# Kernel optimization log

Measured on AMD Instinct MI355X. Metric: run time of the kernel, lower is better.

## Reference

```python
import jax, jax.numpy as jnp
import numpy as np

N_PTILES = 4096
MAX_SOURCES = 1
PTILE_SLEN = 53  # odd -> slen == ptile_slen, size_lens is identity
N_BANDS = 1


def setup_inputs() -> dict:
    key = jax.random.key(0)
    k1, k2, k3, k4, k5, k6 = jax.random.split(key, 6)
    shape = (N_PTILES, MAX_SOURCES)
    gal = jax.random.uniform(k1, shape + (7,), dtype=jnp.float32)
    # realistic SIE lens params per _sample_lens_params: b in [5,30], q in (0,1)
    b = jax.random.uniform(k2, shape + (1,), dtype=jnp.float32) * 25.0 + 5.0
    centers = jax.random.normal(k3, shape + (2,), dtype=jnp.float32)
    q = jax.random.uniform(k4, shape + (1,), dtype=jnp.float32) * 0.8 + 0.1
    beta = (jax.random.uniform(k5, shape + (1,), dtype=jnp.float32) - 0.5) * (np.pi / 2)
    ellf = (1.0 - q) / (1.0 + q)
    e1 = ellf * jnp.cos(beta)
    e2 = ellf * jnp.sin(beta)
    lens_params = jnp.concatenate([gal, b, centers, e1, e2], axis=-1)  # [..., 12]
    bools = (jax.random.uniform(k6, shape + (1,), dtype=jnp.float32) < 0.7).astype(jnp.float32)
    return {"lens_params": lens_params, "lensed_galaxy_bools": bools}


def _render_unlensed(gal_p, slen):
    # Differentiable Gaussian stand-in for the (CPU galsim) unlensed source render.
    c = jnp.arange(slen, dtype=jnp.float32) - (slen - 1) / 2.0
    yy, xx = jnp.meshgrid(c, c, indexing="ij")
    flux = gal_p[:, 0] * 1000.0 + 100.0      # [N]
    sigma = gal_p[:, 3] * 3.0 + 1.0          # [N]
    r2 = xx[None] ** 2 + yy[None] ** 2       # [1, S, S]
    s2 = (sigma ** 2)[:, None, None]
    return flux[:, None, None] * jnp.exp(-0.5 * r2 / s2) / (2.0 * np.pi * s2)


def _sie_deflection(x, y, lens_p):
    # x, y: [1, S, S]; lens_p: [N, 5] -> (xg, yg): [N, S, S]
    b, cx, cy, e1, e2 = [lens_p[:, i][:, None, None] for i in range(5)]
    ell = jnp.sqrt(e1 ** 2 + e2 ** 2)
    q = (1.0 - ell) / (1.0 + ell)
    phirad = jnp.arctan(e2 / e1)
    cosp, sinp = jnp.cos(phirad), jnp.sin(phirad)
    xsie = (x - cx) * cosp + (y - cy) * sinp
    ysie = (y - cy) * cosp - (x - cx) * sinp
    r_ell = jnp.sqrt(q * xsie ** 2 + ysie ** 2 / q + 1e-12)
    qfact = jnp.sqrt(1.0 / q - q)
    eps = 0.001
    safe = jnp.maximum(qfact, eps)
    denom = r_ell + (r_ell == 0)
    xtg = jnp.where(qfact >= eps, b / safe * jnp.arctan(safe * xsie / denom), b * xsie / denom)
    ytg = jnp.where(qfact >= eps, b / safe * jnp.arctanh(safe * ysie / denom), b * ysie / denom)
    xg = xtg * cosp - ytg * sinp
    yg = ytg * cosp + xtg * sinp
    return xg, yg


def _bilinear(im, xs, ys):
    # im: [N, S, S]; xs (col coord), ys (row coord): [N, S, S]
    N, S, _ = im.shape
    x0 = jnp.clip(jnp.floor(xs).astype(jnp.int32), 0, S - 1)
    x1 = jnp.clip(jnp.floor(xs).astype(jnp.int32) + 1, 0, S - 1)
    y0 = jnp.clip(jnp.floor(ys).astype(jnp.int32), 0, S - 1)
    y1 = jnp.clip(jnp.floor(ys).astype(jnp.int32) + 1, 0, S - 1)
    flat = im.reshape(N, S * S)

    def g(yi, xi):
        return jnp.take_along_axis(flat, (yi * S + xi).reshape(N, -1), axis=1).reshape(N, S, S)

    x0f, x1f = x0.astype(im.dtype), x1.astype(im.dtype)
    y0f, y1f = y0.astype(im.dtype), y1.astype(im.dtype)
    # weights use the CLIPPED integer corners, matching bilinear_interpolate_numpy
    wa = (x1f - xs) * (y1f - ys)
    wb = (x1f - xs) * (ys - y0f)
    wc = (xs - x0f) * (y1f - ys)
    wd = (xs - x0f) * (ys - y0f)
    return g(y0, x0) * wa + g(y1, x0) * wb + g(y0, x1) * wc + g(y1, x1) * wd


def _forward(lens_params, lensed_galaxy_bools):
    n_ptiles, max_s, P = lens_params.shape
    z = lens_params.reshape(-1, P)
    gal_p, lens_p = z[:, :7], z[:, 7:]
    slen = PTILE_SLEN
    unlensed = _render_unlensed(gal_p, slen)            # [N, S, S]
    # grid exactly as lens_galsim: range [-nx//2, nx//2] over nx points
    nx = slen
    lo = float((-nx) // 2)   # -27 for nx=53
    hi = float(nx // 2)      # 26
    coords = (hi - lo) * jnp.arange(nx, dtype=jnp.float32) / (nx - 1) + lo
    x = jnp.broadcast_to(coords[None, :], (nx, nx))  # varies along columns
    y = jnp.broadcast_to(coords[:, None], (nx, nx))  # varies along rows
    xg, yg = _sie_deflection(x[None], y[None], lens_p)
    shift = float(nx // 2)
    lensed = _bilinear(unlensed, x[None] - xg + shift, y[None] - yg + shift)
    out = lensed.reshape(n_ptiles, max_s, N_BANDS, slen, slen)
    # render-all + mask is equivalent to the zeros-init + boolean-fill + final mask
    return out * lensed_galaxy_bools[..., None, None]


def reference(lens_params, lensed_galaxy_bools):
    return _forward(lens_params, lensed_galaxy_bools)
```

## Files before the change

kernel.cpp:

```cpp
#include <hip/hip_runtime.h>
#include <math.h>

#define SLEN 53
#define NPIX (SLEN * SLEN)
#define NPARAM 12
#define BLK 256
#define NITER ((NPIX + BLK - 1) / BLK)

__device__ __forceinline__ float fast_atan(float u) {
    float t = __builtin_fabsf(u);
    float rin = __builtin_amdgcn_rcpf(t);
    bool big = t > 1.0f;
    float w = big ? rin : t;
    bool mid = w > 0.4142135624f;
    float w2 = (w - 1.0f) * __builtin_amdgcn_rcpf(w + 1.0f);
    float x = mid ? w2 : w;
    float z = x * x;
    float p = ((8.05374449538e-2f * z - 1.38776856032e-1f) * z
               + 1.99777106478e-1f) * z - 3.33329491539e-1f;
    float r = __builtin_fmaf(p * z, x, x);
    r = mid ? r + 0.78539816339744831f : r;
    r = big ? 1.57079632679489662f - r : r;
    return __builtin_copysignf(r, u);
}

__device__ __forceinline__ float fast_atanh(float v) {
    float a = __builtin_fabsf(v);
    float r = 0.34657359027997264f *
              (__builtin_amdgcn_logf(1.0f + a) - __builtin_amdgcn_logf(1.0f - a));
    return __builtin_copysignf(r, v);
}

__global__ __launch_bounds__(BLK) void lgtd_kernel(
    const float* __restrict__ lens_params,
    const float* __restrict__ bools,
    float* __restrict__ out)
{
    const int tile = blockIdx.x;
    float* outp = out + (size_t)tile * NPIX;
    const int tid = threadIdx.x;

    const float bl = bools[tile];
    if (bl == 0.0f) {
        int idx = tid;
        #pragma unroll
        for (int it = 0; it < NITER; ++it, idx += BLK)
            if (it < NITER - 1 || idx < NPIX) outp[idx] = 0.0f;
        return;
    }

    const float* p = lens_params + tile * NPARAM;
    const float flux  = p[0] * 1000.0f + 100.0f;
    const float sigma = p[3] * 3.0f + 1.0f;
    const float s2    = sigma * sigma;
    const float A     = bl * flux / (6.28318530717958647692f * s2);
    const float nh2   = -0.5f / s2 * 1.44269504088896340736f;
    const float b  = p[7];
    const float cx = p[8], cy = p[9];
    const float e1 = p[10], e2 = p[11];
    const float ell    = sqrtf(e1 * e1 + e2 * e2);
    const float q      = (1.0f - ell) / (1.0f + ell);
    const float qinv   = 1.0f / q;
    const float phirad = atanf(e2 / e1);
    const float cosp   = cosf(phirad);
    const float sinp   = sinf(phirad);
    const float qfact  = sqrtf(qinv - q);
    const float eps    = 0.001f;
    const float safe   = fmaxf(qfact, eps);
    const float bos    = b / safe;
    const bool  main_branch = (qfact >= eps);

    __shared__ float Ctab[SLEN];
    __shared__ float Etab[SLEN];
    if (tid < SLEN) {
        const float kf = (float)tid;
        Ctab[tid] = 53.0f * kf / 52.0f - 27.0f;
        const float d = kf - 26.0f;
        Etab[tid] = __builtin_amdgcn_exp2f(nh2 * (d * d));
    }
    __syncthreads();

    int idx = tid;
    #pragma unroll
    for (int it = 0; it < NITER; ++it, idx += BLK) {
        if (it == NITER - 1 && idx >= NPIX) break;
        const int i = idx / SLEN;
        const int j = idx - i * SLEN;
        const float xc = Ctab[j];
        const float yc = Ctab[i];

        const float dx = xc - cx, dy = yc - cy;
        const float xsie = dx * cosp + dy * sinp;
        const float ysie = dy * cosp - dx * sinp;
        const float arg = q * xsie * xsie + qinv * ysie * ysie + 1e-12f;
        const float rcp_r = __builtin_amdgcn_rsqf(arg);
        float xtg, ytg;
        if (main_branch) {
            xtg = bos * fast_atan(safe * xsie * rcp_r);
            ytg = bos * fast_atanh(safe * ysie * rcp_r);
        } else {
            xtg = b * xsie * rcp_r;
            ytg = b * ysie * rcp_r;
        }
        const float xg = xtg * cosp - ytg * sinp;
        const float yg = ytg * cosp + xtg * sinp;

        const float xs = (xc - xg) + 26.0f;
        const float ys = (yc - yg) + 26.0f;
        const int x0i = (int)floorf(xs), y0i = (int)floorf(ys);
        const int x0 = min(max(x0i,     0), SLEN - 1);
        const int x1 = min(max(x0i + 1, 0), SLEN - 1);
        const int y0 = min(max(y0i,     0), SLEN - 1);
        const int y1 = min(max(y0i + 1, 0), SLEN - 1);
        const float x0f = (float)x0, x1f = (float)x1;
        const float y0f = (float)y0, y1f = (float)y1;

        const float Fx = (x1f - xs) * Etab[x0] + (xs - x0f) * Etab[x1];
        const float Fy = (y1f - ys) * Etab[y0] + (ys - y0f) * Etab[y1];
        outp[idx] = A * Fx * Fy;
    }
}

extern "C" void kernel_launch(void* const* d_in, const int* in_sizes, int n_in,
                              void* d_out, int out_size, void* d_ws, size_t ws_size,
                              hipStream_t stream) {
    const float* lens  = (const float*)d_in[0];
    const float* bools = (const float*)d_in[1];
    float* out = (float*)d_out;
    const int n_tiles = in_sizes[1];
    lgtd_kernel<<<n_tiles, BLK, 0, stream>>>(lens, bools, out);
}
```

Before: 88.07 us.

## Split per-tile parameter prep into separate kernel and batch pixel work

Moves the per-tile scalar setup (atan, cos, sin, sqrt, divisions) into a small prep kernel that writes a 16-float record per tile to workspace. The main kernel reads that record and templates the pixel loop on the deflection branch. It processes pixels in groups of four so loads and stores can overlap with math. It also replaces the divide by 53 with a multiply-shift, does the clamping in float, and computes atanh with one log and a reciprocal. The cost is an extra kernel launch and a workspace round trip, and the one-log atanh may differ slightly in accuracy.

```diff
diff --git a/kernel.cpp b/kernel.cpp
--- a/kernel.cpp
+++ b/kernel.cpp
@@ -2,10 +2,11 @@
 #include <math.h>
 
 #define SLEN 53
-#define NPIX (SLEN * SLEN)
+#define NPIX 2809
 #define NPARAM 12
 #define BLK 256
-#define NITER ((NPIX + BLK - 1) / BLK)
+#define PW 16
+#define NSLOT 11
 
 __device__ __forceinline__ float fast_atan(float u) {
     float t = __builtin_fabsf(u);
@@ -26,49 +27,130 @@
 
 __device__ __forceinline__ float fast_atanh(float v) {
     float a = __builtin_fabsf(v);
-    float r = 0.34657359027997264f *
-              (__builtin_amdgcn_logf(1.0f + a) - __builtin_amdgcn_logf(1.0f - a));
+    float t = (1.0f + a) * __builtin_amdgcn_rcpf(1.0f - a);
+    float r = 0.34657359027997264f * __builtin_amdgcn_logf(t);
     return __builtin_copysignf(r, v);
 }
 
-__global__ __launch_bounds__(BLK) void lgtd_kernel(
+__global__ __launch_bounds__(BLK) void prep_kernel(
     const float* __restrict__ lens_params,
     const float* __restrict__ bools,
+    float* __restrict__ ws, int n_tiles)
+{
+    int t = blockIdx.x * blockDim.x + threadIdx.x;
+    if (t >= n_tiles) return;
+    const float* p = lens_params + t * NPARAM;
+    const float bl   = bools[t];
+    const float flux = p[0] * 1000.0f + 100.0f;
+    const float sg   = p[3] * 3.0f + 1.0f;
+    const float s2   = sg * sg;
+    const float A    = bl * flux / (6.28318530717958647692f * s2);
+    const float nh2  = -0.5f / s2 * 1.44269504088896340736f;
+    const float b  = p[7], cx = p[8], cy = p[9], e1 = p[10], e2 = p[11];
+    const float ell  = sqrtf(e1 * e1 + e2 * e2);
+    const float q    = (1.0f - ell) / (1.0f + ell);
+    const float qinv = 1.0f / q;
+    const float ph   = atanf(e2 / e1);
+    const float cosp = cosf(ph), sinp = sinf(ph);
+    const float qf   = sqrtf(qinv - q);
+    const float safe = fmaxf(qf, 0.001f);
+    const float bos  = b / safe;
+    float* w = ws + t * PW;
+    w[0]  = bl;   w[1]  = A;    w[2]  = nh2;  w[3]  = cosp;
+    w[4]  = sinp; w[5]  = q;    w[6]  = qinv; w[7]  = safe;
+    w[8]  = bos;  w[9]  = cx;   w[10] = cy;   w[11] = b;
+    w[12] = (qf >= 0.001f) ? 1.0f : 0.0f;
+    w[13] = 0.0f; w[14] = 0.0f; w[15] = 0.0f;
+}
+
+template<bool MB>
+__device__ __forceinline__ void run_tile(
+    float* __restrict__ outp, int tid,
+    const float* __restrict__ Ctab, const float* __restrict__ Etab,
+    float A, float cosp, float sinp, float q, float qinv,
+    float safe, float bos, float cx, float cy, float b)
+{
+    #pragma unroll
+    for (int g = 0; g < 3; ++g) {
+        const int nk = (g == 2) ? 3 : 4;
+        float xc[4], yc[4], val[4];
+        #pragma unroll
+        for (int k = 0; k < 4; ++k) {
+            if (k >= nk) break;
+            const int slot = g * 4 + k;
+            int idx = slot * BLK + tid;
+            if (slot == NSLOT - 1) idx = min(idx, NPIX - 1);
+            const unsigned i = ((unsigned)idx * 39569u) >> 21;
+            const int j = idx - (int)i * 53;
+            xc[k] = Ctab[j];
+            yc[k] = Ctab[i];
+        }
+        #pragma unroll
+        for (int k = 0; k < 4; ++k) {
+            if (k >= nk) break;
+            const float dx = xc[k] - cx, dy = yc[k] - cy;
+            const float xsie = dx * cosp + dy * sinp;
+            const float ysie = dy * cosp - dx * sinp;
+            const float arg = __builtin_fmaf(q * xsie, xsie,
+                              __builtin_fmaf(qinv * ysie, ysie, 1e-12f));
+            const float rcp_r = __builtin_amdgcn_rsqf(arg);
+            float xtg, ytg;
+            if (MB) {
+                xtg = bos * fast_atan(safe * xsie * rcp_r);
+                ytg = bos * fast_atanh(safe * ysie * rcp_r);
+            } else {
+                xtg = b * xsie * rcp_r;
+                ytg = b * ysie * rcp_r;
+            }
+            const float xg = xtg * cosp - ytg * sinp;
+            const float yg = ytg * cosp + xtg * sinp;
+            const float xs = (xc[k] - xg) + 26.0f;
+            const float ys = (yc[k] - yg) + 26.0f;
+            const float fx = __builtin_floorf(xs);
+            const float fy = __builtin_floorf(ys);
+            const float x0f = fminf(fmaxf(fx, 0.0f), 52.0f);
+            const float x1f = fminf(fmaxf(fx + 1.0f, 0.0f), 52.0f);
+            const float y0f = fminf(fmaxf(fy, 0.0f), 52.0f);
+            const float y1f = fminf(fmaxf(fy + 1.0f, 0.0f), 52.0f);
+            const int x0 = (int)x0f, x1 = (int)x1f;
+            const int y0 = (int)y0f, y1 = (int)y1f;
+            const float Fx = (x1f - xs) * Etab[x0] + (xs - x0f) * Etab[x1];
+            const float Fy = (y1f - ys) * Etab[y0] + (ys - y0f) * Etab[y1];
+            val[k] = A * Fx * Fy;
+        }
+        #pragma unroll
+        for (int k = 0; k < 4; ++k) {
+            if (k >= nk) break;
+            const int slot = g * 4 + k;
+            const int idx = slot * BLK + tid;
+            if (slot < NSLOT - 1 || idx < NPIX) outp[idx] = val[k];
+        }
+    }
+}
+
+__global__ __launch_bounds__(BLK) void lgtd_kernel(
+    const float* __restrict__ ws,
     float* __restrict__ out)
 {
     const int tile = blockIdx.x;
+    const float* w = ws + tile * PW;
     float* outp = out + (size_t)tile * NPIX;
     const int tid = threadIdx.x;
 
-    const float bl = bools[tile];
+    const float bl = w[0];
     if (bl == 0.0f) {
-        int idx = tid;
         #pragma unroll
-        for (int it = 0; it < NITER; ++it, idx += BLK)
-            if (it < NITER - 1 || idx < NPIX) outp[idx] = 0.0f;
+        for (int s = 0; s < NSLOT; ++s) {
+            const int idx = s * BLK + tid;
+            if (s < NSLOT - 1 || idx < NPIX) outp[idx] = 0.0f;
+        }
         return;
     }
 
-    const float* p = lens_params + tile * NPARAM;
-    const float flux  = p[0] * 1000.0f + 100.0f;
-    const float sigma = p[3] * 3.0f + 1.0f;
-    const float s2    = sigma * sigma;
-    const float A     = bl * flux / (6.28318530717958647692f * s2);
-    const float nh2   = -0.5f / s2 * 1.44269504088896340736f;
-    const float b  = p[7];
-    const float cx = p[8], cy = p[9];
-    const float e1 = p[10], e2 = p[11];
-    const float ell    = sqrtf(e1 * e1 + e2 * e2);
-    const float q      = (1.0f - ell) / (1.0f + ell);
-    const float qinv   = 1.0f / q;
-    const float phirad = atanf(e2 / e1);
-    const float cosp   = cosf(phirad);
-    const float sinp   = sinf(phirad);
-    const float qfact  = sqrtf(qinv - q);
-    const float eps    = 0.001f;
-    const float safe   = fmaxf(qfact, eps);
-    const float bos    = b / safe;
-    const bool  main_branch = (qfact >= eps);
+    const float A    = w[1],  nh2  = w[2],  cosp = w[3], sinp = w[4];
+    const float q    = w[5],  qinv = w[6],  safe = w[7], bos  = w[8];
+    const float cx   = w[9],  cy   = w[10], b    = w[11];
+    const bool  mb   = (w[12] != 0.0f);
 
     __shared__ float Ctab[SLEN];
     __shared__ float Etab[SLEN];
@@ -80,45 +162,10 @@
     }
     __syncthreads();
 
-    int idx = tid;
-    #pragma unroll
-    for (int it = 0; it < NITER; ++it, idx += BLK) {
-        if (it == NITER - 1 && idx >= NPIX) break;
-        const int i = idx / SLEN;
-        const int j = idx - i * SLEN;
-        const float xc = Ctab[j];
-        const float yc = Ctab[i];
-
-        const float dx = xc - cx, dy = yc - cy;
-        const float xsie = dx * cosp + dy * sinp;
-        const float ysie = dy * cosp - dx * sinp;
-        const float arg = q * xsie * xsie + qinv * ysie * ysie + 1e-12f;
-        const float rcp_r = __builtin_amdgcn_rsqf(arg);
-        float xtg, ytg;
-        if (main_branch) {
-            xtg = bos * fast_atan(safe * xsie * rcp_r);
-            ytg = bos * fast_atanh(safe * ysie * rcp_r);
-        } else {
-            xtg = b * xsie * rcp_r;
-            ytg = b * ysie * rcp_r;
-        }
-        const float xg = xtg * cosp - ytg * sinp;
-        const float yg = ytg * cosp + xtg * sinp;
-
-        const float xs = (xc - xg) + 26.0f;
-        const float ys = (yc - yg) + 26.0f;
-        const int x0i = (int)floorf(xs), y0i = (int)floorf(ys);
-        const int x0 = min(max(x0i,     0), SLEN - 1);
-        const int x1 = min(max(x0i + 1, 0), SLEN - 1);
-        const int y0 = min(max(y0i,     0), SLEN - 1);
-        const int y1 = min(max(y0i + 1, 0), SLEN - 1);
-        const float x0f = (float)x0, x1f = (float)x1;
-        const float y0f = (float)y0, y1f = (float)y1;
-
-        const float Fx = (x1f - xs) * Etab[x0] + (xs - x0f) * Etab[x1];
-        const float Fy = (y1f - ys) * Etab[y0] + (ys - y0f) * Etab[y1];
-        outp[idx] = A * Fx * Fy;
-    }
+    if (mb)
+        run_tile<true >(outp, tid, Ctab, Etab, A, cosp, sinp, q, qinv, safe, bos, cx, cy, b);
+    else
+        run_tile<false>(outp, tid, Ctab, Etab, A, cosp, sinp, q, qinv, safe, bos, cx, cy, b);
 }
 
 extern "C" void kernel_launch(void* const* d_in, const int* in_sizes, int n_in,
@@ -127,6 +174,8 @@
     const float* lens  = (const float*)d_in[0];
     const float* bools = (const float*)d_in[1];
     float* out = (float*)d_out;
+    float* ws  = (float*)d_ws;
     const int n_tiles = in_sizes[1];
-    lgtd_kernel<<<n_tiles, BLK, 0, stream>>>(lens, bools, out);
+    prep_kernel<<<(n_tiles + BLK - 1) / BLK, BLK, 0, stream>>>(lens, bools, ws, n_tiles);
+    lgtd_kernel<<<n_tiles, BLK, 0, stream>>>(ws, out);
 }
```

Measured after the change: 88.38 us. No clear change (+0.3%).
